# Kernel tuning notes

Hardware: AMD Instinct MI355X
Metric: run time of the kernel (lower is better)

The kernel has to match this reference:

```python
import jax, jax.numpy as jnp
import numpy as np

S, B, E = 2048, 2, 1024
H = 16
HD = E // H
RANK = 8
ALPHA = 16.0
LORA_SCALE = ALPHA / RANK


def setup_inputs() -> dict:
    key = jax.random.key(0)
    ks = jax.random.split(key, 13)
    d = {
        'query': jax.random.normal(ks[0], (S, B, E), jnp.float32),
        'key': jax.random.normal(ks[1], (S, B, E), jnp.float32),
        'value': jax.random.normal(ks[2], (S, B, E), jnp.float32),
        'in_proj_weight': jax.random.normal(ks[3], (3 * E, E), jnp.float32) * 0.02,
        'in_proj_bias': jax.random.normal(ks[4], (3 * E,), jnp.float32) * 0.02,
        'out_w': jax.random.normal(ks[5], (E, E), jnp.float32) * 0.02,
        'out_b': jax.random.normal(ks[6], (E,), jnp.float32) * 0.02,
        'A_q': jax.random.normal(ks[7], (RANK, E), jnp.float32) * 0.02,
        'B_q': jax.random.normal(ks[8], (E, RANK), jnp.float32) * 0.02,
        'A_k': jax.random.normal(ks[9], (RANK, E), jnp.float32) * 0.02,
        'B_k': jax.random.normal(ks[10], (E, RANK), jnp.float32) * 0.02,
        'A_v': jax.random.normal(ks[11], (RANK, E), jnp.float32) * 0.02,
        'B_v': jax.random.normal(ks[12], (E, RANK), jnp.float32) * 0.02,
    }
    return d


def _proj(x, W, b, A, Bm):
    # frozen linear + LoRA low-rank delta: x @ W.T + b + ((x @ A.T) @ B.T) * scale
    base = jnp.einsum('sbe,fe->sbf', x, W) + b
    lora = jnp.einsum('sbr,fr->sbf', jnp.einsum('sbe,re->sbr', x, A), Bm) * LORA_SCALE
    return base + lora


def reference(query, key, value, in_proj_weight, in_proj_bias, out_w, out_b,
              A_q, B_q, A_k, B_k, A_v, B_v):
    Wq, Wk, Wv = in_proj_weight[:E], in_proj_weight[E:2 * E], in_proj_weight[2 * E:]
    bq, bk, bv = in_proj_bias[:E], in_proj_bias[E:2 * E], in_proj_bias[2 * E:]
    q = _proj(query, Wq, bq, A_q, B_q)   # [S,B,E]
    k = _proj(key, Wk, bk, A_k, B_k)
    v = _proj(value, Wv, bv, A_v, B_v)
    # reshape to [B*H, S, HD] (seq-first layout, matching torch view/transpose)
    def heads(x):
        return x.reshape(S, B * H, HD).transpose(1, 0, 2)
    qh, kh, vh = heads(q), heads(k), heads(v)
    scale = HD ** -0.5
    attn = jnp.einsum('nsd,ntd->nst', qh, kh) * scale  # [B*H,S,S]
    attn = jax.nn.softmax(attn, axis=-1)
    out = jnp.einsum('nst,ntd->nsd', attn, vh)         # [B*H,S,HD]
    out = out.transpose(1, 0, 2).reshape(S, B, E)
    out = jnp.einsum('sbe,fe->sbf', out, out_w) + out_b
    return out
```

## Files before the change

### kernel.cpp

```cpp
#include <hip/hip_runtime.h>
#include <stdint.h>

static const int S_ = 2048, B_ = 2, E_ = 1024, H_ = 16, HD_ = 64, MR_ = 4096;

typedef __bf16 bf16;
typedef __bf16 bf16x8 __attribute__((ext_vector_type(8)));
typedef float  f32x4  __attribute__((ext_vector_type(4)));
typedef float  f32x16 __attribute__((ext_vector_type(16)));
typedef unsigned short u16x8 __attribute__((ext_vector_type(8)));

#define AS1(p) ((const __attribute__((address_space(1))) void*)(p))
#define AS3(p) ((__attribute__((address_space(3))) void*)(p))

#define QSCALE 0.18033688011112042f

static __device__ __forceinline__ uint32_t cvtpk_bf16(float lo, float hi) {
    uint32_t r;
    asm("v_cvt_pk_bf16_f32 %0, %1, %2" : "=v"(r) : "v"(lo), "v"(hi));
    return r;
}

__global__ __launch_bounds__(256) void cvt_all(const float* __restrict__ s0,
                                               const float* __restrict__ s1,
                                               const float* __restrict__ s2,
                                               const float* __restrict__ s3,
                                               bf16* __restrict__ d0,
                                               bf16* __restrict__ d1,
                                               bf16* __restrict__ d2,
                                               bf16* __restrict__ d3) {
    int b = blockIdx.x;
    const float* src;
    bf16* dst;
    int i;
    if (b < 6144) {
        int seg = b >> 11;
        i = (b & 2047) * 256 + threadIdx.x;
        src = seg == 0 ? s0 : (seg == 1 ? s1 : s2);
        dst = seg == 0 ? d0 : (seg == 1 ? d1 : d2);
    } else {
        i = (b - 6144) * 256 + threadIdx.x;
        src = s3; dst = d3;
    }
    const float4* s = (const float4*)src;
    float4 a = s[i * 2], c = s[i * 2 + 1];
    bf16x8 v;
    v[0] = (bf16)a.x; v[1] = (bf16)a.y; v[2] = (bf16)a.z; v[3] = (bf16)a.w;
    v[4] = (bf16)c.x; v[5] = (bf16)c.y; v[6] = (bf16)c.z; v[7] = (bf16)c.w;
    *(bf16x8*)(dst + (size_t)i * 8) = v;
}

__global__ __launch_bounds__(256) void build_weff3(const float* __restrict__ W,
                                                   const float* __restrict__ A0,
                                                   const float* __restrict__ B0,
                                                   const float* __restrict__ A1,
                                                   const float* __restrict__ B1,
                                                   const float* __restrict__ A2,
                                                   const float* __restrict__ B2,
                                                   bf16* __restrict__ o0,
                                                   bf16* __restrict__ o1,
                                                   bf16* __restrict__ o2) {
    int z = blockIdx.y;
    const float* A = z == 0 ? A0 : (z == 1 ? A1 : A2);
    const float* Bm = z == 0 ? B0 : (z == 1 ? B1 : B2);
    bf16* out = z == 0 ? o0 : (z == 1 ? o1 : o2);
    const float* Wz = W + (size_t)z * 1024 * 1024;
    int idx = blockIdx.x * 256 + threadIdx.x;
    int f = idx >> 10, e = idx & 1023;
    float acc = Wz[idx];
#pragma unroll
    for (int r = 0; r < 8; r++) acc += 2.0f * Bm[f * 8 + r] * A[r * 1024 + e];
    out[idx] = (bf16)acc;
}

__global__ __launch_bounds__(256) void gemm_qkv(const bf16* __restrict__ XQ,
                                                const bf16* __restrict__ XK,
                                                const bf16* __restrict__ XV,
                                                const bf16* __restrict__ WQ,
                                                const bf16* __restrict__ WK,
                                                const bf16* __restrict__ WV,
                                                const float* __restrict__ ipb,
                                                bf16* __restrict__ QH,
                                                bf16* __restrict__ KH,
                                                bf16* __restrict__ VH) {
    int z = blockIdx.z;
    const bf16* Amat = z == 0 ? XQ : (z == 1 ? XK : XV);
    const bf16* Bmat = z == 0 ? WQ : (z == 1 ? WK : WV);
    bf16* Cout = z == 0 ? QH : (z == 1 ? KH : VH);
    const float* bias = ipb + z * 1024;
    float cscale = z == 0 ? QSCALE : 1.0f;

    __shared__ bf16 smbuf[16896];
    const int tid = threadIdx.x;
    const int wid = tid >> 6, lane = tid & 63;
    const int lg = lane >> 4, li = lane & 15;
    const int m0 = blockIdx.y * 128, n0 = blockIdx.x * 128;
    const int wr = wid >> 1, wc = wid & 1;

    f32x4 acc[4][4] = {};

    for (int kt = 0; kt < 1024; kt += 64) {
        __syncthreads();
#pragma unroll
        for (int h = 0; h < 2; h++)
#pragma unroll
            for (int i = 0; i < 2; i++) {
                int c = wid * 2 + i;
                const bf16* ga = Amat + (size_t)(m0 + c * 16 + (lane >> 2)) * 1024 + kt + h * 32 + (lane & 3) * 8;
                __builtin_amdgcn_global_load_lds(AS1(ga), AS3(smbuf + h * 4096 + c * 512), 16, 0, 0);
                const bf16* gb = Bmat + (size_t)(n0 + c * 16 + (lane >> 2)) * 1024 + kt + h * 32 + (lane & 3) * 8;
                __builtin_amdgcn_global_load_lds(AS1(gb), AS3(smbuf + 8192 + h * 4096 + c * 512), 16, 0, 0);
            }
        __syncthreads();

#pragma unroll
        for (int h = 0; h < 2; h++) {
            bf16x8 a[4], b[4];
#pragma unroll
            for (int mi = 0; mi < 4; mi++)
                a[mi] = *(const bf16x8*)(smbuf + h * 4096 + (wr * 64 + mi * 16 + li) * 32 + lg * 8);
#pragma unroll
            for (int ni = 0; ni < 4; ni++)
                b[ni] = *(const bf16x8*)(smbuf + 8192 + h * 4096 + (wc * 64 + ni * 16 + li) * 32 + lg * 8);
#pragma unroll
            for (int mi = 0; mi < 4; mi++)
#pragma unroll
                for (int ni = 0; ni < 4; ni++)
                    acc[mi][ni] = __builtin_amdgcn_mfma_f32_16x16x32_bf16(a[mi], b[ni], acc[mi][ni], 0, 0, 0);
        }
    }

    __syncthreads();
#pragma unroll
    for (int ni = 0; ni < 4; ni++) {
        int fl = wc * 64 + ni * 16 + li;
        float bv = bias[n0 + fl];
#pragma unroll
        for (int mi = 0; mi < 4; mi++)
#pragma unroll
            for (int r = 0; r < 4; r++) {
                int ml_ = wr * 64 + mi * 16 + lg * 4 + r;
                smbuf[ml_ * 132 + fl] = (bf16)((acc[mi][ni][r] + bv) * cscale);
            }
    }
    __syncthreads();
#pragma unroll
    for (int k = 0; k < 8; k++) {
        int c = tid + 256 * k;
        int dhalf = c & 7, m = (c >> 3) & 127, hl = c >> 10;
        u16x8 v = *(const u16x8*)(smbuf + m * 132 + hl * 64 + dhalf * 8);
        int mg = m0 + m, fg = n0 + hl * 64;
        int s = mg >> 1, bb = mg & 1, h = fg >> 6, d = dhalf * 8;
        *(u16x8*)(Cout + (size_t)(bb * 16 + h) * S_ * 64 + (size_t)s * 64 + d) = v;
    }
}

__global__ __launch_bounds__(256) void gemm_out64(const bf16* __restrict__ Amat,
                                                  const bf16* __restrict__ Bmat,
                                                  const float* __restrict__ bias,
                                                  float* __restrict__ Cout) {
    __shared__ bf16 Asm[2][64 * 32];
    __shared__ bf16 Bsm[2][128 * 32];
    const int tid = threadIdx.x;
    const int wid = tid >> 6, lane = tid & 63;
    const int lg = lane >> 4, li = lane & 15;
    const int m0 = blockIdx.y * 64, n0 = blockIdx.x * 128;
    const int wr = wid >> 1, wc = wid & 1;

    f32x4 acc[2][4] = {};

    for (int kt = 0; kt < 1024; kt += 64) {
        __syncthreads();
#pragma unroll
        for (int h = 0; h < 2; h++)
            for (int j = wid; j < 12; j += 4) {
                if (j < 4) {
                    const bf16* ga = Amat + (size_t)(m0 + j * 16 + (lane >> 2)) * 1024 + kt + h * 32 + (lane & 3) * 8;
                    __builtin_amdgcn_global_load_lds(AS1(ga), AS3(&Asm[h][j * 512]), 16, 0, 0);
                } else {
                    int c = j - 4;
                    const bf16* gb = Bmat + (size_t)(n0 + c * 16 + (lane >> 2)) * 1024 + kt + h * 32 + (lane & 3) * 8;
                    __builtin_amdgcn_global_load_lds(AS1(gb), AS3(&Bsm[h][c * 512]), 16, 0, 0);
                }
            }
        __syncthreads();

#pragma unroll
        for (int h = 0; h < 2; h++) {
            bf16x8 a[2], b[4];
#pragma unroll
            for (int mi = 0; mi < 2; mi++)
                a[mi] = *(const bf16x8*)(&Asm[h][(wr * 32 + mi * 16 + li) * 32 + lg * 8]);
#pragma unroll
            for (int ni = 0; ni < 4; ni++)
                b[ni] = *(const bf16x8*)(&Bsm[h][(wc * 64 + ni * 16 + li) * 32 + lg * 8]);
#pragma unroll
            for (int mi = 0; mi < 2; mi++)
#pragma unroll
                for (int ni = 0; ni < 4; ni++)
                    acc[mi][ni] = __builtin_amdgcn_mfma_f32_16x16x32_bf16(a[mi], b[ni], acc[mi][ni], 0, 0, 0);
        }
    }

#pragma unroll
    for (int ni = 0; ni < 4; ni++) {
        int f = n0 + wc * 64 + ni * 16 + li;
        float bv = bias[f];
#pragma unroll
        for (int mi = 0; mi < 2; mi++)
#pragma unroll
            for (int r = 0; r < 4; r++) {
                int m = m0 + wr * 32 + mi * 16 + lg * 4 + r;
                Cout[(size_t)m * 1024 + f] = acc[mi][ni][r] + bv;
            }
    }
}

__global__ __launch_bounds__(256, 4) void attn_fwd(const bf16* __restrict__ qh,
                                                   const bf16* __restrict__ kh,
                                                   const bf16* __restrict__ vh,
                                                   bf16* __restrict__ outbuf) {
    __shared__ __attribute__((aligned(16))) char smem[33280];

    const int bid = blockIdx.x;
    const int head = (bid & 7) * 4 + ((bid >> 3) & 3);
    const int qt = bid >> 5;
    const int tid = threadIdx.x, wid = tid >> 6, l = tid & 63;
    const int li = l & 31, hi = l >> 5;
    const int kvh = wid & 1;

    const bf16* Qb = qh + (size_t)head * S_ * 64;
    const bf16* Kb = kh + (size_t)head * S_ * 64;
    const bf16* Vb = vh + (size_t)head * S_ * 64;
    const int q0 = qt * 64 + (wid >> 1) * 32;

    bf16x8 qf[4];
#pragma unroll
    for (int s = 0; s < 4; s++)
        qf[s] = *(const bf16x8*)(Qb + (size_t)(q0 + li) * 64 + 16 * s + 8 * hi);

    f32x16 oacc0 = {}, oacc1 = {};
    float lsum = 0.f;

    const int krow = tid >> 3, kc = tid & 7;
    const int kswz = 16 * (krow & 7);
    const int vk2 = tid & 31, vdb = (tid >> 5) * 8;
    const int rswz = 16 * (li & 7);

    u16x8 kreg0, kreg1, vreg0, vreg1;
    kreg0 = *(const u16x8*)(Kb + (size_t)krow * 64 + 8 * kc);
    kreg1 = *(const u16x8*)(Kb + (size_t)(krow + 32) * 64 + 8 * kc);
    vreg0 = *(const u16x8*)(Vb + (size_t)(2 * vk2) * 64 + vdb);
    vreg1 = *(const u16x8*)(Vb + (size_t)(2 * vk2 + 1) * 64 + vdb);

    for (int t = 0; t < 32; t++) {
        const int cur = t & 1;
        char* Kc = smem + cur * 8192;
        char* Vc = smem + 16384 + cur * 8192;
        *(u16x8*)(Kc + krow * 128 + ((16 * kc) ^ kswz)) = kreg0;
        *(u16x8*)(Kc + (krow + 32) * 128 + ((16 * kc) ^ kswz)) = kreg1;
#pragma unroll
        for (int i = 0; i < 8; i++) {
            uint32_t w = (uint32_t)vreg0[i] | ((uint32_t)vreg1[i] << 16);
            *(uint32_t*)(Vc + (vdb + i) * 128 + ((4 * vk2) ^ (16 * i))) = w;
        }
        __syncthreads();
        if (t + 1 < 32) {
            int kv0 = (t + 1) * 64;
            kreg0 = *(const u16x8*)(Kb + (size_t)(kv0 + krow) * 64 + 8 * kc);
            kreg1 = *(const u16x8*)(Kb + (size_t)(kv0 + krow + 32) * 64 + 8 * kc);
            vreg0 = *(const u16x8*)(Vb + (size_t)(kv0 + 2 * vk2) * 64 + vdb);
            vreg1 = *(const u16x8*)(Vb + (size_t)(kv0 + 2 * vk2 + 1) * 64 + vdb);
        }

        f32x16 s = {};
        __builtin_amdgcn_s_setprio(1);
#pragma unroll
        for (int step = 0; step < 4; step++) {
            bf16x8 k0 = *(const bf16x8*)(Kc + (kvh * 32 + li) * 128 + ((32 * step + 16 * hi) ^ rswz));
            s = __builtin_amdgcn_mfma_f32_32x32x16_bf16(k0, qf[step], s, 0, 0, 0);
        }
        __builtin_amdgcn_s_setprio(0);

        bf16x8 pa[2];
#pragma unroll
        for (int g = 0; g < 2; g++) {
            float p[8];
#pragma unroll
            for (int i = 0; i < 8; i++) {
                p[i] = __builtin_amdgcn_exp2f(s[8 * g + i]);
                lsum += p[i];
            }
            uint32_t w0 = cvtpk_bf16(p[0], p[1]);
            uint32_t w1 = cvtpk_bf16(p[2], p[3]);
            uint32_t w2 = cvtpk_bf16(p[4], p[5]);
            uint32_t w3 = cvtpk_bf16(p[6], p[7]);
            uint32_t sa = hi ? w0 : w2;
            uint32_t sb = hi ? w1 : w3;
            uint32_t ea = (uint32_t)__shfl_xor((int)sa, 32);
            uint32_t eb = (uint32_t)__shfl_xor((int)sb, 32);
            union { uint32_t u[4]; bf16x8 v; } pu;
            pu.u[0] = hi ? ea : w0;
            pu.u[1] = hi ? eb : w1;
            pu.u[2] = hi ? w2 : ea;
            pu.u[3] = hi ? w3 : eb;
            pa[g] = pu.v;
        }

        __builtin_amdgcn_s_setprio(1);
#pragma unroll
        for (int g = 0; g < 2; g++) {
            int kvb = 64 * kvh + 32 * g + 16 * hi;
            bf16x8 v0 = *(const bf16x8*)(Vc + li * 128 + (kvb ^ rswz));
            oacc0 = __builtin_amdgcn_mfma_f32_32x32x16_bf16(pa[g], v0, oacc0, 0, 0, 0);
            bf16x8 v1 = *(const bf16x8*)(Vc + (32 + li) * 128 + (kvb ^ rswz));
            oacc1 = __builtin_amdgcn_mfma_f32_32x32x16_bf16(pa[g], v1, oacc1, 0, 0, 0);
        }
        __builtin_amdgcn_s_setprio(0);
    }

    __syncthreads();
    float* mlp = (float*)(smem + 32768);
    float* scr = (float*)smem;
    float lt = lsum + __shfl_xor(lsum, 32);
    if (l < 32) mlp[wid * 32 + l] = lt;
    {
        float* mys = scr + wid * 1024;
#pragma unroll
        for (int r = 0; r < 16; r++) {
            int rp = (r & 3) + 8 * (r >> 2) + 4 * hi;
            mys[rp * 32 + li] = kvh ? oacc0[r] : oacc1[r];
        }
    }
    __syncthreads();
    float pl = mlp[(wid ^ 1) * 32 + li];
    float linv = 1.0f / (lt + pl);
    const float* ps = scr + (wid ^ 1) * 1024;
    int bb = head >> 4, h = head & 15;
#pragma unroll
    for (int r = 0; r < 16; r++) {
        int rp = (r & 3) + 8 * (r >> 2) + 4 * hi;
        int q = q0 + rp;
        float own = kvh ? oacc1[r] : oacc0[r];
        float part = ps[rp * 32 + li];
        float val = (own + part) * __shfl(linv, rp);
        outbuf[(size_t)(q * 2 + bb) * 1024 + h * 64 + kvh * 32 + li] = (bf16)val;
    }
}

extern "C" void kernel_launch(void* const* d_in, const int* in_sizes, int n_in,
                              void* d_out, int out_size, void* d_ws, size_t ws_size,
                              hipStream_t stream) {
    const float* query = (const float*)d_in[0];
    const float* key_  = (const float*)d_in[1];
    const float* value = (const float*)d_in[2];
    const float* ipw   = (const float*)d_in[3];
    const float* ipb   = (const float*)d_in[4];
    const float* out_w = (const float*)d_in[5];
    const float* out_b = (const float*)d_in[6];
    const float* A_q   = (const float*)d_in[7];
    const float* B_q   = (const float*)d_in[8];
    const float* A_k   = (const float*)d_in[9];
    const float* B_k   = (const float*)d_in[10];
    const float* A_v   = (const float*)d_in[11];
    const float* B_v   = (const float*)d_in[12];

    const size_t MB = 1ull << 20;
    if (ws_size < 64 * MB) return;
    char* ws = (char*)d_ws;
    bf16* XQ = (bf16*)(ws + 0 * MB);
    bf16* XK = (bf16*)(ws + 8 * MB);
    bf16* XV = (bf16*)(ws + 16 * MB);
    bf16* WQ = (bf16*)(ws + 24 * MB);
    bf16* WK = (bf16*)(ws + 26 * MB);
    bf16* WV = (bf16*)(ws + 28 * MB);
    bf16* WO = (bf16*)(ws + 30 * MB);
    bf16* QH = (bf16*)(ws + 32 * MB);
    bf16* KH = (bf16*)(ws + 40 * MB);
    bf16* VH = (bf16*)(ws + 48 * MB);
    bf16* AT = (bf16*)(ws + 56 * MB);

    cvt_all<<<6656, 256, 0, stream>>>(query, key_, value, out_w, XQ, XK, XV, WO);
    build_weff3<<<dim3(4096, 3), 256, 0, stream>>>(ipw, A_q, B_q, A_k, B_k, A_v, B_v,
                                                   WQ, WK, WV);

    gemm_qkv<<<dim3(8, 32, 3), 256, 0, stream>>>(XQ, XK, XV, WQ, WK, WV, ipb, QH, KH, VH);

    attn_fwd<<<1024, 256, 0, stream>>>(QH, KH, VH, AT);

    gemm_out64<<<dim3(8, 64), 256, 0, stream>>>(AT, WO, out_b, (float*)d_out);
}
```

Before: 138.7 us.

## Stage K via global_load_lds and use 32x32x8 MFMA to skip P shuffles

K tiles are now loaded straight from global memory into LDS with global_load_lds and a pre-swizzled source offset, replacing the register round trip and ds_write. The P·V step switches to the older 32x32x8 bf16 MFMA, whose operand layout matches the QK accumulator layout. This removes the cross-half shfl_xor permutation of P, and the V LDS swizzle is changed to suit the narrower 8-byte reads. The trade-off is twice as many PV MFMA instructions issued through inline asm, which the compiler cannot schedule around as freely.

```diff
diff --git a/kernel.cpp b/kernel.cpp
--- a/kernel.cpp
+++ b/kernel.cpp
@@ -8,6 +8,7 @@
 typedef float  f32x4  __attribute__((ext_vector_type(4)));
 typedef float  f32x16 __attribute__((ext_vector_type(16)));
 typedef unsigned short u16x8 __attribute__((ext_vector_type(8)));
+typedef short  s16x4  __attribute__((ext_vector_type(4)));
 
 #define AS1(p) ((const __attribute__((address_space(1))) void*)(p))
 #define AS3(p) ((__attribute__((address_space(3))) void*)(p))
@@ -241,35 +242,42 @@
     f32x16 oacc0 = {}, oacc1 = {};
     float lsum = 0.f;
 
-    const int krow = tid >> 3, kc = tid & 7;
-    const int kswz = 16 * (krow & 7);
+    const size_t kg_off = ((size_t)(16 * (l & 7)) ^ (16 * ((l >> 3) & 7)));
     const int vk2 = tid & 31, vdb = (tid >> 5) * 8;
     const int rswz = 16 * (li & 7);
-
-    u16x8 kreg0, kreg1, vreg0, vreg1;
-    kreg0 = *(const u16x8*)(Kb + (size_t)krow * 64 + 8 * kc);
-    kreg1 = *(const u16x8*)(Kb + (size_t)(krow + 32) * 64 + 8 * kc);
+    const int vswz = 8 * (li & 15);
+
+#define STAGE_K(kv0, dstbuf)                                                    \
+    {                                                                           \
+        _Pragma("unroll")                                                       \
+        for (int j = 0; j < 2; j++) {                                           \
+            int row = (j * 4 + wid) * 8 + (l >> 3);                             \
+            const char* srcp = (const char*)Kb + (size_t)((kv0) + row) * 128 + kg_off; \
+            __builtin_amdgcn_global_load_lds(AS1(srcp),                         \
+                AS3((dstbuf) + (j * 4 + wid) * 1024), 16, 0, 0);                \
+        }                                                                       \
+    }
+
+    u16x8 vreg0, vreg1;
     vreg0 = *(const u16x8*)(Vb + (size_t)(2 * vk2) * 64 + vdb);
     vreg1 = *(const u16x8*)(Vb + (size_t)(2 * vk2 + 1) * 64 + vdb);
+    STAGE_K(0, smem);
 
     for (int t = 0; t < 32; t++) {
         const int cur = t & 1;
         char* Kc = smem + cur * 8192;
         char* Vc = smem + 16384 + cur * 8192;
-        *(u16x8*)(Kc + krow * 128 + ((16 * kc) ^ kswz)) = kreg0;
-        *(u16x8*)(Kc + (krow + 32) * 128 + ((16 * kc) ^ kswz)) = kreg1;
 #pragma unroll
         for (int i = 0; i < 8; i++) {
             uint32_t w = (uint32_t)vreg0[i] | ((uint32_t)vreg1[i] << 16);
-            *(uint32_t*)(Vc + (vdb + i) * 128 + ((4 * vk2) ^ (16 * i))) = w;
+            *(uint32_t*)(Vc + (vdb + i) * 128 + ((4 * vk2) ^ (8 * ((vdb + i) & 15)))) = w;
         }
         __syncthreads();
         if (t + 1 < 32) {
             int kv0 = (t + 1) * 64;
-            kreg0 = *(const u16x8*)(Kb + (size_t)(kv0 + krow) * 64 + 8 * kc);
-            kreg1 = *(const u16x8*)(Kb + (size_t)(kv0 + krow + 32) * 64 + 8 * kc);
             vreg0 = *(const u16x8*)(Vb + (size_t)(kv0 + 2 * vk2) * 64 + vdb);
             vreg1 = *(const u16x8*)(Vb + (size_t)(kv0 + 2 * vk2 + 1) * 64 + vdb);
+            STAGE_K(kv0, smem + (cur ^ 1) * 8192);
         }
 
         f32x16 s = {};
@@ -281,39 +289,32 @@
         }
         __builtin_amdgcn_s_setprio(0);
 
-        bf16x8 pa[2];
-#pragma unroll
-        for (int g = 0; g < 2; g++) {
-            float p[8];
-#pragma unroll
-            for (int i = 0; i < 8; i++) {
-                p[i] = __builtin_amdgcn_exp2f(s[8 * g + i]);
-                lsum += p[i];
-            }
-            uint32_t w0 = cvtpk_bf16(p[0], p[1]);
-            uint32_t w1 = cvtpk_bf16(p[2], p[3]);
-            uint32_t w2 = cvtpk_bf16(p[4], p[5]);
-            uint32_t w3 = cvtpk_bf16(p[6], p[7]);
-            uint32_t sa = hi ? w0 : w2;
-            uint32_t sb = hi ? w1 : w3;
-            uint32_t ea = (uint32_t)__shfl_xor((int)sa, 32);
-            uint32_t eb = (uint32_t)__shfl_xor((int)sb, 32);
-            union { uint32_t u[4]; bf16x8 v; } pu;
-            pu.u[0] = hi ? ea : w0;
-            pu.u[1] = hi ? eb : w1;
-            pu.u[2] = hi ? w2 : ea;
-            pu.u[3] = hi ? w3 : eb;
-            pa[g] = pu.v;
+        float p[16];
+#pragma unroll
+        for (int r = 0; r < 16; r++) {
+            p[r] = __builtin_amdgcn_exp2f(s[r]);
+            lsum += p[r];
+        }
+        s16x4 pa[4];
+#pragma unroll
+        for (int st = 0; st < 4; st++) {
+            uint32_t w0 = cvtpk_bf16(p[4 * st], p[4 * st + 1]);
+            uint32_t w1 = cvtpk_bf16(p[4 * st + 2], p[4 * st + 3]);
+            union { uint32_t u[2]; s16x4 v; } pu;
+            pu.u[0] = w0; pu.u[1] = w1;
+            pa[st] = pu.v;
         }
 
         __builtin_amdgcn_s_setprio(1);
 #pragma unroll
-        for (int g = 0; g < 2; g++) {
-            int kvb = 64 * kvh + 32 * g + 16 * hi;
-            bf16x8 v0 = *(const bf16x8*)(Vc + li * 128 + (kvb ^ rswz));
-            oacc0 = __builtin_amdgcn_mfma_f32_32x32x16_bf16(pa[g], v0, oacc0, 0, 0, 0);
-            bf16x8 v1 = *(const bf16x8*)(Vc + (32 + li) * 128 + (kvb ^ rswz));
-            oacc1 = __builtin_amdgcn_mfma_f32_32x32x16_bf16(pa[g], v1, oacc1, 0, 0, 0);
+        for (int st = 0; st < 4; st++) {
+            int byteoff = (64 * kvh + 16 * st + 8 * hi) ^ vswz;
+            s16x4 v0 = *(const s16x4*)(Vc + li * 128 + byteoff);
+            s16x4 v1 = *(const s16x4*)(Vc + (32 + li) * 128 + byteoff);
+            asm("v_mfma_f32_32x32x8_bf16 %0, %1, %2, %0"
+                : "+v"(oacc0) : "v"(pa[st]), "v"(v0));
+            asm("v_mfma_f32_32x32x8_bf16 %0, %1, %2, %0"
+                : "+v"(oacc1) : "v"(pa[st]), "v"(v1));
         }
         __builtin_amdgcn_s_setprio(0);
     }
```

After: 140.1 us. About the same (+1.0%).
